# Optimization experiments

Measured on AMD Instinct MI355X. Metric: run time of the kernel, lower is better.

## Reference

```python
import jax, jax.numpy as jnp
import numpy as np

B, IN, E, H, MO, OUT, K = 32768, 512, 8, 128, 256, 2, 2


def setup_inputs() -> dict:
    key = jax.random.key(0)
    ks = jax.random.split(key, 9)
    g = lambda k, shape, fan: (jax.random.normal(k, shape, jnp.float32) / np.sqrt(fan)).astype(jnp.float32)
    return {
        "num_prop": jax.random.normal(ks[0], (B, IN), jnp.float32),
        "cat_prop": jax.random.normal(ks[1], (B, 3), jnp.float32),
        "w_gate": g(ks[2], (IN, E), IN),
        "W1": g(ks[3], (E, IN, H), IN),
        "b1": jnp.zeros((E, H), jnp.float32),
        "W2": g(ks[4], (E, H, MO), H),
        "b2": jnp.zeros((E, MO), jnp.float32),
        "Wout": g(ks[5], (MO, OUT), MO),
        "bout": jnp.zeros((OUT,), jnp.float32),
    }


def _cv_squared(v):
    # torch.var is unbiased (ddof=1); eps = 1e-10
    return jnp.var(v, ddof=1) / (jnp.mean(v) ** 2 + 1e-10)


def reference(num_prop, cat_prop, w_gate, W1, b1, W2, b2, Wout, bout):
    b = num_prop.shape[0]
    x = num_prop  # eval mode: dropout is identity, gating noise disabled
    # --- top-k gating ---
    logits = x @ w_gate                                   # [B, E]
    top_vals, top_idx = jax.lax.top_k(logits, K)          # [B, K]
    gate_vals = jax.nn.softmax(top_vals, axis=-1)         # softmax over top-k logits
    gates = jnp.zeros_like(logits).at[jnp.arange(b)[:, None], top_idx].add(gate_vals)  # [B, E]
    # --- load-balancing loss ---
    importance = gates.sum(axis=0)                        # [E]
    load = (gates > 0).astype(jnp.float32).sum(axis=0)    # [E]
    loss = (_cv_squared(importance) + _cv_squared(load)) * 1e-2
    # --- experts (dense-equivalent: gates zero out non-selected experts) ---
    h = jax.nn.relu(jnp.einsum('bi,eih->beh', x, W1) + b1)          # [B, E, H]
    eo = jax.nn.softmax(jnp.einsum('beh,ehm->bem', h, W2) + b2, axis=-1)  # [B, E, MO]
    y = jnp.einsum('be,bem->bm', gates, eo)               # [B, MO]
    # --- output head ---
    out = y @ Wout + bout                                 # [B, OUT]
    return out, loss
```

## Files before the change

### kernel.cpp

```cpp
#include <hip/hip_runtime.h>

#define BN 32768
#define IN 512
#define NE 8
#define NH 128
#define MO 256

typedef const __attribute__((address_space(1))) unsigned int gu32;
typedef __attribute__((address_space(3))) unsigned int lu32;
typedef __attribute__((ext_vector_type(8))) short bf16x8;
typedef __attribute__((ext_vector_type(4))) float f32x4;

__device__ __forceinline__ void cp16(const float* g, float* l) {
    __builtin_amdgcn_global_load_lds((gu32*)g, (lu32*)l, 16, 0, 0);
}

__device__ __forceinline__ unsigned short f2bf(float f) {
    unsigned int u = __float_as_uint(f);
    u = (u + 0x7fffu + ((u >> 16) & 1u)) >> 16;
    return (unsigned short)u;
}
__device__ __forceinline__ float bf2f(unsigned short h) {
    return __uint_as_float((unsigned int)h << 16);
}

__global__ __launch_bounds__(256) void gate_kernel(
    const float* __restrict__ x, const float* __restrict__ wg,
    int* __restrict__ gcount, int* __restrict__ gload, float* __restrict__ gimp,
    int* __restrict__ idx_list, float* __restrict__ gate_list,
    float* __restrict__ out, const float* __restrict__ bout)
{
    __shared__ double wgt[NE][514];
    __shared__ int counts_s[NE];
    __shared__ int load_s[NE];
    __shared__ float imp_s[NE];
    __shared__ int base_s[NE];
    __shared__ int rec_e[64];
    __shared__ int rec_p[64];
    __shared__ float rec_g[64];

    int tid = threadIdx.x;
    if (tid < NE) { counts_s[tid] = 0; load_s[tid] = 0; imp_s[tid] = 0.f; }
    if (tid < 64) {
        int row = blockIdx.x * 32 + (tid >> 1);
        out[row * 2 + (tid & 1)] = bout[tid & 1];
    }
    for (int i = tid; i < IN * NE; i += 256) {
        wgt[i & 7][i >> 3] = (double)wg[i];
    }
    __syncthreads();

    int r = tid >> 3;
    int e = tid & 7;
    int row = blockIdx.x * 32 + r;

    const float4* x4 = (const float4*)(x + (size_t)row * IN);
    const double* wrow = &wgt[e][0];
    double a0 = 0.0, a1 = 0.0, a2 = 0.0, a3 = 0.0;
    #pragma unroll 8
    for (int j = 0; j < 128; ++j) {
        float4 xv = x4[j];
        const double2* wd = (const double2*)(wrow + 4 * j);
        double2 w0 = wd[0];
        double2 w1 = wd[1];
        a0 = fma((double)xv.x, w0.x, a0);
        a1 = fma((double)xv.y, w0.y, a1);
        a2 = fma((double)xv.z, w1.x, a2);
        a3 = fma((double)xv.w, w1.y, a3);
    }
    double acc = (a0 + a1) + (a2 + a3);

    double v0 = acc; int e0 = e;
    #pragma unroll
    for (int m = 1; m < 8; m <<= 1) {
        double vo = __shfl_xor(v0, m, 64);
        int    eo = __shfl_xor(e0, m, 64);
        if (vo > v0 || (vo == v0 && eo < e0)) { v0 = vo; e0 = eo; }
    }
    double v1 = (e == e0) ? -1.0e300 : acc; int e1 = e;
    #pragma unroll
    for (int m = 1; m < 8; m <<= 1) {
        double vo = __shfl_xor(v1, m, 64);
        int    eo = __shfl_xor(e1, m, 64);
        if (vo > v1 || (vo == v1 && eo < e1)) { v1 = vo; e1 = eo; }
    }

    if ((tid & 7) == 0) {
        float t1 = expf((float)(v1 - v0));
        float s = 1.f + t1;
        float g0 = 1.f / s;
        float g1 = t1 / s;
        atomicAdd(&imp_s[e0], g0);
        atomicAdd(&imp_s[e1], g1);
        if (g0 > 0.f) atomicAdd(&load_s[e0], 1);
        if (g1 > 0.f) atomicAdd(&load_s[e1], 1);
        int p0 = atomicAdd(&counts_s[e0], 1);
        int p1 = atomicAdd(&counts_s[e1], 1);
        int rl = r * 2;
        rec_e[rl] = e0; rec_e[rl + 1] = e1;
        rec_g[rl] = g0; rec_g[rl + 1] = g1;
        rec_p[rl] = p0; rec_p[rl + 1] = p1;
    }
    __syncthreads();
    if (tid < NE) {
        base_s[tid] = atomicAdd(&gcount[tid], counts_s[tid]);
        atomicAdd(&gimp[tid], imp_s[tid]);
        atomicAdd(&gload[tid], load_s[tid]);
    }
    __syncthreads();
    if (tid < 64) {
        int ee = rec_e[tid];
        int pos = base_s[ee] + rec_p[tid];
        int rw = blockIdx.x * 32 + (tid >> 1);
        idx_list[ee * BN + pos] = rw;
        gate_list[ee * BN + pos] = rec_g[tid];
    }
}

__global__ void loss_kernel(const float* __restrict__ gimp, const int* __restrict__ gload,
                            float* __restrict__ out) {
    if (threadIdx.x == 0 && blockIdx.x == 0) {
        float mi = 0.f, ml = 0.f;
        for (int e = 0; e < NE; ++e) { mi += gimp[e]; ml += (float)gload[e]; }
        mi *= 0.125f; ml *= 0.125f;
        float vi = 0.f, vl = 0.f;
        for (int e = 0; e < NE; ++e) {
            float d = gimp[e] - mi;  vi += d * d;
            float d2 = (float)gload[e] - ml; vl += d2 * d2;
        }
        vi *= (1.f / 7.f); vl *= (1.f / 7.f);
        float loss = (vi / (mi * mi + 1e-10f) + vl / (ml * ml + 1e-10f)) * 0.01f;
        out[BN * 2] = loss;
    }
}

__global__ __launch_bounds__(256) void prep_kernel(
    const float* __restrict__ W1, const float* __restrict__ W2,
    float* __restrict__ W1F, float* __restrict__ W2F)
{
    __shared__ __align__(16) char pb[32768];
    int t = threadIdx.x, b = blockIdx.x;
    if (b < 64) {
        int e = b >> 3, kt = b & 7;
        const float* src = W1 + ((size_t)e * IN + kt * 64) * NH;
        #pragma unroll
        for (int p = 0; p < 8; ++p) {
            int li = p * 256 + t;
            float4 q = *(const float4*)(src + li * 4);
            int kl = li >> 5, n0 = (li & 31) * 4;
            int ks = kl >> 5, g = (kl >> 3) & 3, kb = (kl & 7) * 2;
            float vv[4] = {q.x, q.y, q.z, q.w};
            #pragma unroll
            for (int j = 0; j < 4; ++j) {
                int n = n0 + j;
                int off = (((ks * 8 + (n >> 4)) * 64) + (n & 15) + 16 * g) * 16 + kb;
                unsigned short hh = f2bf(vv[j]);
                unsigned short hl = f2bf(vv[j] - bf2f(hh));
                *(unsigned short*)(pb + off) = hh;
                *(unsigned short*)(pb + 16384 + off) = hl;
            }
        }
        __syncthreads();
        float* dst = W1F + (size_t)b * 8192;
        #pragma unroll
        for (int p = 0; p < 8; ++p) {
            int li = p * 256 + t;
            *(int4*)(dst + li * 4) = *(const int4*)(pb + li * 16);
        }
    } else if (b < 96) {
        int bi = b - 64;
        int e = bi >> 2, kt = bi & 3;
        const float* src = W2 + ((size_t)e * NH + kt * 32) * MO;
        #pragma unroll
        for (int p = 0; p < 8; ++p) {
            int li = p * 256 + t;
            float4 q = *(const float4*)(src + li * 4);
            int kl = li >> 6, n0 = (li & 63) * 4;
            int g = kl >> 3, kb = (kl & 7) * 2;
            float vv[4] = {q.x, q.y, q.z, q.w};
            #pragma unroll
            for (int j = 0; j < 4; ++j) {
                int n = n0 + j;
                int off = ((n >> 4) * 64 + (n & 15) + 16 * g) * 16 + kb;
                unsigned short hh = f2bf(vv[j]);
                unsigned short hl = f2bf(vv[j] - bf2f(hh));
                *(unsigned short*)(pb + off) = hh;
                *(unsigned short*)(pb + 16384 + off) = hl;
            }
        }
        __syncthreads();
        float* dst = W2F + (size_t)bi * 8192;
        #pragma unroll
        for (int p = 0; p < 8; ++p) {
            int li = p * 256 + t;
            *(int4*)(dst + li * 4) = *(const int4*)(pb + li * 16);
        }
    }
}

#define OFF_AH 0
#define OFF_AL 8192
#define OFF_B1 16384
#define OFF_HH 0
#define OFF_HL 16384
#define OFF_B2 32768

__global__ __launch_bounds__(256, 2) void expert_kernel(
    const float* __restrict__ x,
    const float* __restrict__ b1, const float* __restrict__ b2,
    const float* __restrict__ Wout,
    const float* __restrict__ W1F, const float* __restrict__ W2F,
    const int* __restrict__ gcount,
    const int* __restrict__ idx_list, const float* __restrict__ gate_list,
    float* __restrict__ out)
{
    __shared__ __align__(16) char smx[66560];
    __shared__ float woutS[512];

    int e = blockIdx.y;
    int cnt = gcount[e];
    int row0 = blockIdx.x * 64;
    if (row0 >= cnt) return;
    int t = threadIdx.x;
    int l = t & 63, w = t >> 6;

    woutS[t] = Wout[t];
    woutS[256 + t] = Wout[256 + t];

    int s_mf = t >> 6;
    int s_r  = t & 15;
    int s_g  = (t >> 4) & 3;
    int rloc = s_mf * 16 + s_r;
    int sgi = row0 + rloc; if (sgi >= cnt) sgi = cnt - 1;
    const float* xrow = x + (size_t)idx_list[e * BN + sgi] * IN;

    int mbase = (w & 1) * 2;
    int nsel  = w >> 1;

    f32x4 acc1[2][4] = {};
    for (int kt = 0; kt < 8; ++kt) {
        {
            const float* gb = W1F + (size_t)(e * 8 + kt) * 8192;
            float* lb = (float*)(smx + OFF_B1);
            #pragma unroll
            for (int p = 0; p < 8; ++p)
                cp16(gb + (p * 256 + t) * 4, lb + (p * 256 + t) * 4);
        }
        #pragma unroll
        for (int ks = 0; ks < 2; ++ks) {
            int k = kt * 64 + ks * 32 + s_g * 8;
            float4 qa = *(const float4*)(xrow + k);
            float4 qb = *(const float4*)(xrow + k + 4);
            float vv[8] = {qa.x, qa.y, qa.z, qa.w, qb.x, qb.y, qb.z, qb.w};
            unsigned int dh[4], dl[4];
            #pragma unroll
            for (int j = 0; j < 4; ++j) {
                unsigned short h0 = f2bf(vv[2 * j]);
                unsigned short h1 = f2bf(vv[2 * j + 1]);
                unsigned short l0 = f2bf(vv[2 * j] - bf2f(h0));
                unsigned short l1 = f2bf(vv[2 * j + 1] - bf2f(h1));
                dh[j] = (unsigned int)h0 | ((unsigned int)h1 << 16);
                dl[j] = (unsigned int)l0 | ((unsigned int)l1 << 16);
            }
            int slot = ((ks * 4 + s_mf) * 64 + (s_r + 16 * s_g)) * 16;
            *(int4*)(smx + OFF_AH + slot) = make_int4(dh[0], dh[1], dh[2], dh[3]);
            *(int4*)(smx + OFF_AL + slot) = make_int4(dl[0], dl[1], dl[2], dl[3]);
        }
        __syncthreads();
        #pragma unroll
        for (int ks = 0; ks < 2; ++ks) {
            bf16x8 ah[2], al[2];
            #pragma unroll
            for (int mf = 0; mf < 2; ++mf) {
                int ao = ((ks * 4 + mbase + mf) * 64 + l) * 16;
                ah[mf] = *(const bf16x8*)(smx + OFF_AH + ao);
                al[mf] = *(const bf16x8*)(smx + OFF_AL + ao);
            }
            #pragma unroll
            for (int nf = 0; nf < 4; ++nf) {
                int bo = ((ks * 8 + nsel * 4 + nf) * 64 + l) * 16;
                bf16x8 bh = *(const bf16x8*)(smx + OFF_B1 + bo);
                bf16x8 bl = *(const bf16x8*)(smx + OFF_B1 + 16384 + bo);
                #pragma unroll
                for (int mf = 0; mf < 2; ++mf) {
                    acc1[mf][nf] = __builtin_amdgcn_mfma_f32_16x16x32_bf16(ah[mf], bh, acc1[mf][nf], 0, 0, 0);
                    acc1[mf][nf] = __builtin_amdgcn_mfma_f32_16x16x32_bf16(ah[mf], bl, acc1[mf][nf], 0, 0, 0);
                    acc1[mf][nf] = __builtin_amdgcn_mfma_f32_16x16x32_bf16(al[mf], bh, acc1[mf][nf], 0, 0, 0);
                    acc1[mf][nf] = __builtin_amdgcn_mfma_f32_16x16x32_bf16(al[mf], bl, acc1[mf][nf], 0, 0, 0);
                }
            }
        }
        __syncthreads();
    }

    #pragma unroll
    for (int mf = 0; mf < 2; ++mf) {
        int mf2 = (w & 1) * 2 + mf;
        int rlow = 4 * (l >> 4);
        #pragma unroll
        for (int nf = 0; nf < 4; ++nf) {
            int c = nsel * 64 + nf * 16 + (l & 15);
            float b1v = b1[e * NH + c];
            int ks2 = c >> 5;
            int g2 = (c >> 3) & 3;
            int boff = ((ks2 * 4 + mf2) * 64) * 16 + (c & 7) * 2;
            #pragma unroll
            for (int rg = 0; rg < 4; ++rg) {
                float v = fmaxf(acc1[mf][nf][rg] + b1v, 0.f);
                unsigned short hh = f2bf(v);
                unsigned short hl = f2bf(v - bf2f(hh));
                int off = boff + ((rlow + rg) + 16 * g2) * 16;
                *(unsigned short*)(smx + OFF_HH + off) = hh;
                *(unsigned short*)(smx + OFF_HL + off) = hl;
            }
        }
    }
    __syncthreads();

    f32x4 acc2[2][8] = {};
    for (int kt2 = 0; kt2 < 4; ++kt2) {
        {
            const float* gb = W2F + (size_t)(e * 4 + kt2) * 8192;
            float* lb = (float*)(smx + OFF_B2);
            #pragma unroll
            for (int p = 0; p < 8; ++p)
                cp16(gb + (p * 256 + t) * 4, lb + (p * 256 + t) * 4);
        }
        __syncthreads();
        bf16x8 ah[2], al[2];
        #pragma unroll
        for (int mf = 0; mf < 2; ++mf) {
            int ao = ((kt2 * 4 + mbase + mf) * 64 + l) * 16;
            ah[mf] = *(const bf16x8*)(smx + OFF_HH + ao);
            al[mf] = *(const bf16x8*)(smx + OFF_HL + ao);
        }
        #pragma unroll
        for (int nf = 0; nf < 8; ++nf) {
            int bo = ((nsel * 8 + nf) * 64 + l) * 16;
            bf16x8 bh = *(const bf16x8*)(smx + OFF_B2 + bo);
            bf16x8 bl = *(const bf16x8*)(smx + OFF_B2 + 16384 + bo);
            #pragma unroll
            for (int mf = 0; mf < 2; ++mf) {
                acc2[mf][nf] = __builtin_amdgcn_mfma_f32_16x16x32_bf16(ah[mf], bh, acc2[mf][nf], 0, 0, 0);
                acc2[mf][nf] = __builtin_amdgcn_mfma_f32_16x16x32_bf16(ah[mf], bl, acc2[mf][nf], 0, 0, 0);
                acc2[mf][nf] = __builtin_amdgcn_mfma_f32_16x16x32_bf16(al[mf], bh, acc2[mf][nf], 0, 0, 0);
                acc2[mf][nf] = __builtin_amdgcn_mfma_f32_16x16x32_bf16(al[mf], bl, acc2[mf][nf], 0, 0, 0);
            }
        }
        __syncthreads();
    }

    float* zl = (float*)smx;
    #pragma unroll
    for (int mf = 0; mf < 2; ++mf) {
        int rbase = (w & 1) * 32 + mf * 16 + 4 * (l >> 4);
        #pragma unroll
        for (int nf = 0; nf < 8; ++nf) {
            int c = nsel * 128 + nf * 16 + (l & 15);
            float b2v = b2[e * MO + c];
            #pragma unroll
            for (int rg = 0; rg < 4; ++rg)
                zl[(rbase + rg) * 260 + c] = acc2[mf][nf][rg] + b2v;
        }
    }
    __syncthreads();

    int rr = w * 16 + (l >> 2);
    int c0 = l & 3;
    float vreg[64];
    float m = -1e30f;
    #pragma unroll
    for (int j = 0; j < 64; ++j) {
        vreg[j] = zl[rr * 260 + c0 + 4 * j];
        m = fmaxf(m, vreg[j]);
    }
    m = fmaxf(m, __shfl_xor(m, 1, 64));
    m = fmaxf(m, __shfl_xor(m, 2, 64));
    float s = 0.f, o0 = 0.f, o1 = 0.f;
    #pragma unroll
    for (int j = 0; j < 64; ++j) {
        float tt = __expf(vreg[j] - m);
        s += tt;
        float2 wv = *(const float2*)&woutS[(c0 + 4 * j) * 2];
        o0 = fmaf(tt, wv.x, o0);
        o1 = fmaf(tt, wv.y, o1);
    }
    s  += __shfl_xor(s, 1, 64);  s  += __shfl_xor(s, 2, 64);
    o0 += __shfl_xor(o0, 1, 64); o0 += __shfl_xor(o0, 2, 64);
    o1 += __shfl_xor(o1, 1, 64); o1 += __shfl_xor(o1, 2, 64);
    if (c0 == 0) {
        int gi = row0 + rr;
        if (gi < cnt) {
            float g = gate_list[e * BN + gi];
            int brow = idx_list[e * BN + gi];
            float inv = 1.f / s;
            atomicAdd(&out[brow * 2 + 0], g * o0 * inv);
            atomicAdd(&out[brow * 2 + 1], g * o1 * inv);
        }
    }
}

extern "C" void kernel_launch(void* const* d_in, const int* in_sizes, int n_in,
                              void* d_out, int out_size, void* d_ws, size_t ws_size,
                              hipStream_t stream) {
    const float* x    = (const float*)d_in[0];
    const float* wg   = (const float*)d_in[2];
    const float* W1   = (const float*)d_in[3];
    const float* b1   = (const float*)d_in[4];
    const float* W2   = (const float*)d_in[5];
    const float* b2   = (const float*)d_in[6];
    const float* Wout = (const float*)d_in[7];
    const float* bout = (const float*)d_in[8];
    float* out = (float*)d_out;

    char* ws = (char*)d_ws;
    int*   gcount    = (int*)(ws + 0);
    int*   gload     = (int*)(ws + 32);
    float* gimp      = (float*)(ws + 64);
    int*   idx_list  = (int*)(ws + 128);
    float* gate_list = (float*)(ws + 128 + sizeof(int) * NE * BN);
    float* W1F       = (float*)(ws + 128 + 8 * NE * BN);
    float* W2F       = (float*)(ws + 128 + 8 * NE * BN + 64 * 32768);

    hipMemsetAsync(ws, 0, 128, stream);
    prep_kernel<<<96, 256, 0, stream>>>(W1, W2, W1F, W2F);
    gate_kernel<<<BN / 32, 256, 0, stream>>>(x, wg, gcount, gload, gimp,
                                             idx_list, gate_list, out, bout);
    loss_kernel<<<1, 64, 0, stream>>>(gimp, gload, out);
    dim3 eg(BN / 64, NE);
    expert_kernel<<<eg, 256, 0, stream>>>(x, b1, b2, Wout, W1F, W2F,
                                          gcount, idx_list, gate_list, out);
}
```

Measured before the change: 228.0 us.

## Compute gating logits with split-bf16 MFMA, FP64 fallback for near-ties; fold loss into expert kernel

The gate kernel now computes logits with split-bf16 MFMA (hi/lo parts, three products) instead of per-thread FP64 dot products, covering 64 rows per block. When the 2nd and 3rd logits are within a small margin, it recomputes that row in FP64 so the top-2 selection still matches. The separate loss kernel is removed and its work done by one thread of the expert kernel, saving a launch. The risks are divergent slow paths when near-ties occur, and the tie threshold being too small to catch every MFMA rounding error.

```diff
diff --git a/kernel.cpp b/kernel.cpp
--- a/kernel.cpp
+++ b/kernel.cpp
@@ -30,76 +30,135 @@
     int* __restrict__ idx_list, float* __restrict__ gate_list,
     float* __restrict__ out, const float* __restrict__ bout)
 {
-    __shared__ double wgt[NE][514];
+    __shared__ __align__(16) char wb[32768];
     __shared__ int counts_s[NE];
     __shared__ int load_s[NE];
     __shared__ float imp_s[NE];
     __shared__ int base_s[NE];
-    __shared__ int rec_e[64];
-    __shared__ int rec_p[64];
-    __shared__ float rec_g[64];
+    __shared__ int rec_e[128];
+    __shared__ int rec_p[128];
+    __shared__ float rec_g[128];
 
     int tid = threadIdx.x;
     if (tid < NE) { counts_s[tid] = 0; load_s[tid] = 0; imp_s[tid] = 0.f; }
-    if (tid < 64) {
-        int row = blockIdx.x * 32 + (tid >> 1);
+    if (tid < 128) {
+        int row = blockIdx.x * 64 + (tid >> 1);
         out[row * 2 + (tid & 1)] = bout[tid & 1];
     }
-    for (int i = tid; i < IN * NE; i += 256) {
-        wgt[i & 7][i >> 3] = (double)wg[i];
+    for (int idx = tid; idx < 1024; idx += 256) {
+        int ks = idx >> 6, ls = idx & 63;
+        int col = ls & 15;
+        int kb = 32 * ks + 8 * (ls >> 4);
+        unsigned int ph[4], pl[4];
+        #pragma unroll
+        for (int j = 0; j < 4; ++j) {
+            float v0 = (col < 8) ? wg[(kb + 2 * j) * NE + col] : 0.f;
+            float v1 = (col < 8) ? wg[(kb + 2 * j + 1) * NE + col] : 0.f;
+            unsigned short h0 = f2bf(v0), h1 = f2bf(v1);
+            unsigned short l0 = f2bf(v0 - bf2f(h0)), l1 = f2bf(v1 - bf2f(h1));
+            ph[j] = (unsigned int)h0 | ((unsigned int)h1 << 16);
+            pl[j] = (unsigned int)l0 | ((unsigned int)l1 << 16);
+        }
+        *(int4*)(wb + ks * 1024 + ls * 16) = make_int4(ph[0], ph[1], ph[2], ph[3]);
+        *(int4*)(wb + 16384 + ks * 1024 + ls * 16) = make_int4(pl[0], pl[1], pl[2], pl[3]);
     }
     __syncthreads();
 
-    int r = tid >> 3;
-    int e = tid & 7;
-    int row = blockIdx.x * 32 + r;
-
-    const float4* x4 = (const float4*)(x + (size_t)row * IN);
-    const double* wrow = &wgt[e][0];
-    double a0 = 0.0, a1 = 0.0, a2 = 0.0, a3 = 0.0;
-    #pragma unroll 8
-    for (int j = 0; j < 128; ++j) {
-        float4 xv = x4[j];
-        const double2* wd = (const double2*)(wrow + 4 * j);
-        double2 w0 = wd[0];
-        double2 w1 = wd[1];
-        a0 = fma((double)xv.x, w0.x, a0);
-        a1 = fma((double)xv.y, w0.y, a1);
-        a2 = fma((double)xv.z, w1.x, a2);
-        a3 = fma((double)xv.w, w1.y, a3);
-    }
-    double acc = (a0 + a1) + (a2 + a3);
-
-    double v0 = acc; int e0 = e;
-    #pragma unroll
-    for (int m = 1; m < 8; m <<= 1) {
-        double vo = __shfl_xor(v0, m, 64);
-        int    eo = __shfl_xor(e0, m, 64);
-        if (vo > v0 || (vo == v0 && eo < e0)) { v0 = vo; e0 = eo; }
-    }
-    double v1 = (e == e0) ? -1.0e300 : acc; int e1 = e;
-    #pragma unroll
-    for (int m = 1; m < 8; m <<= 1) {
-        double vo = __shfl_xor(v1, m, 64);
-        int    eo = __shfl_xor(e1, m, 64);
-        if (vo > v1 || (vo == v1 && eo < e1)) { v1 = vo; e1 = eo; }
-    }
-
-    if ((tid & 7) == 0) {
-        float t1 = expf((float)(v1 - v0));
-        float s = 1.f + t1;
-        float g0 = 1.f / s;
-        float g1 = t1 / s;
-        atomicAdd(&imp_s[e0], g0);
-        atomicAdd(&imp_s[e1], g1);
-        if (g0 > 0.f) atomicAdd(&load_s[e0], 1);
-        if (g1 > 0.f) atomicAdd(&load_s[e1], 1);
-        int p0 = atomicAdd(&counts_s[e0], 1);
-        int p1 = atomicAdd(&counts_s[e1], 1);
-        int rl = r * 2;
-        rec_e[rl] = e0; rec_e[rl + 1] = e1;
-        rec_g[rl] = g0; rec_g[rl + 1] = g1;
-        rec_p[rl] = p0; rec_p[rl + 1] = p1;
+    int w = tid >> 6, l = tid & 63;
+    int e = l & 15;
+    int rowA = blockIdx.x * 64 + w * 16 + e;
+    const float* px = x + (size_t)rowA * IN + 8 * (l >> 4);
+
+    f32x4 acc = {};
+    #pragma unroll
+    for (int ks = 0; ks < 16; ++ks) {
+        float4 qa = *(const float4*)(px + 32 * ks);
+        float4 qb = *(const float4*)(px + 32 * ks + 4);
+        float v[8] = {qa.x, qa.y, qa.z, qa.w, qb.x, qb.y, qb.z, qb.w};
+        bf16x8 ah, al;
+        #pragma unroll
+        for (int i = 0; i < 8; ++i) {
+            unsigned short h = f2bf(v[i]);
+            ah[i] = (short)h;
+            al[i] = (short)f2bf(v[i] - bf2f(h));
+        }
+        bf16x8 bh = *(const bf16x8*)(wb + ks * 1024 + l * 16);
+        bf16x8 bl = *(const bf16x8*)(wb + 16384 + ks * 1024 + l * 16);
+        acc = __builtin_amdgcn_mfma_f32_16x16x32_bf16(ah, bh, acc, 0, 0, 0);
+        acc = __builtin_amdgcn_mfma_f32_16x16x32_bf16(ah, bl, acc, 0, 0, 0);
+        acc = __builtin_amdgcn_mfma_f32_16x16x32_bf16(al, bh, acc, 0, 0, 0);
+    }
+
+    #pragma unroll
+    for (int reg = 0; reg < 4; ++reg) {
+        int rloc = w * 16 + 4 * (l >> 4) + reg;
+        int row = blockIdx.x * 64 + rloc;
+        float lv = (e < 8) ? acc[reg] : -1e30f;
+
+        float v0 = lv; int e0 = e;
+        #pragma unroll
+        for (int m = 1; m < 8; m <<= 1) {
+            float vo = __shfl_xor(v0, m, 64);
+            int eo = __shfl_xor(e0, m, 64);
+            if (vo > v0 || (vo == v0 && eo < e0)) { v0 = vo; e0 = eo; }
+        }
+        float v1 = (e == e0 || e >= 8) ? -1e30f : lv; int e1 = e;
+        #pragma unroll
+        for (int m = 1; m < 8; m <<= 1) {
+            float vo = __shfl_xor(v1, m, 64);
+            int eo = __shfl_xor(e1, m, 64);
+            if (vo > v1 || (vo == v1 && eo < e1)) { v1 = vo; e1 = eo; }
+        }
+        float v2 = (e == e0 || e == e1 || e >= 8) ? -1e30f : lv;
+        #pragma unroll
+        for (int m = 1; m < 8; m <<= 1) v2 = fmaxf(v2, __shfl_xor(v2, m, 64));
+
+        double dv0 = v0, dv1 = v1;
+        int f0 = e0, f1 = e1;
+        if (e < 8 && v1 - v2 < 2e-4f) {
+            const float* xr = x + (size_t)row * IN;
+            double d0 = 0, d1 = 0, d2 = 0, d3 = 0;
+            for (int k = 0; k < IN; k += 4) {
+                float4 xv = *(const float4*)(xr + k);
+                d0 = fma((double)xv.x, (double)wg[(k    ) * NE + e], d0);
+                d1 = fma((double)xv.y, (double)wg[(k + 1) * NE + e], d1);
+                d2 = fma((double)xv.z, (double)wg[(k + 2) * NE + e], d2);
+                d3 = fma((double)xv.w, (double)wg[(k + 3) * NE + e], d3);
+            }
+            double ad = (d0 + d1) + (d2 + d3);
+            double w0 = ad; int g0i = e;
+            #pragma unroll
+            for (int m = 1; m < 8; m <<= 1) {
+                double vo = __shfl_xor(w0, m, 64);
+                int eo = __shfl_xor(g0i, m, 64);
+                if (vo > w0 || (vo == w0 && eo < g0i)) { w0 = vo; g0i = eo; }
+            }
+            double w1 = (e == g0i) ? -1.0e300 : ad; int g1i = e;
+            #pragma unroll
+            for (int m = 1; m < 8; m <<= 1) {
+                double vo = __shfl_xor(w1, m, 64);
+                int eo = __shfl_xor(g1i, m, 64);
+                if (vo > w1 || (vo == w1 && eo < g1i)) { w1 = vo; g1i = eo; }
+            }
+            dv0 = w0; dv1 = w1; f0 = g0i; f1 = g1i;
+        }
+
+        if (e == 0) {
+            float t1 = expf((float)(dv1 - dv0));
+            float s = 1.f + t1;
+            float g0 = 1.f / s;
+            float g1 = t1 / s;
+            atomicAdd(&imp_s[f0], g0);
+            atomicAdd(&imp_s[f1], g1);
+            if (g0 > 0.f) atomicAdd(&load_s[f0], 1);
+            if (g1 > 0.f) atomicAdd(&load_s[f1], 1);
+            int p0 = atomicAdd(&counts_s[f0], 1);
+            int p1 = atomicAdd(&counts_s[f1], 1);
+            int rl = rloc * 2;
+            rec_e[rl] = f0; rec_e[rl + 1] = f1;
+            rec_g[rl] = g0; rec_g[rl + 1] = g1;
+            rec_p[rl] = p0; rec_p[rl + 1] = p1;
+        }
     }
     __syncthreads();
     if (tid < NE) {
@@ -108,29 +167,12 @@
         atomicAdd(&gload[tid], load_s[tid]);
     }
     __syncthreads();
-    if (tid < 64) {
+    if (tid < 128) {
         int ee = rec_e[tid];
         int pos = base_s[ee] + rec_p[tid];
-        int rw = blockIdx.x * 32 + (tid >> 1);
+        int rw = blockIdx.x * 64 + (tid >> 1);
         idx_list[ee * BN + pos] = rw;
         gate_list[ee * BN + pos] = rec_g[tid];
-    }
-}
-
-__global__ void loss_kernel(const float* __restrict__ gimp, const int* __restrict__ gload,
-                            float* __restrict__ out) {
-    if (threadIdx.x == 0 && blockIdx.x == 0) {
-        float mi = 0.f, ml = 0.f;
-        for (int e = 0; e < NE; ++e) { mi += gimp[e]; ml += (float)gload[e]; }
-        mi *= 0.125f; ml *= 0.125f;
-        float vi = 0.f, vl = 0.f;
-        for (int e = 0; e < NE; ++e) {
-            float d = gimp[e] - mi;  vi += d * d;
-            float d2 = (float)gload[e] - ml; vl += d2 * d2;
-        }
-        vi *= (1.f / 7.f); vl *= (1.f / 7.f);
-        float loss = (vi / (mi * mi + 1e-10f) + vl / (ml * ml + 1e-10f)) * 0.01f;
-        out[BN * 2] = loss;
     }
 }
 
@@ -211,6 +253,7 @@
     const float* __restrict__ Wout,
     const float* __restrict__ W1F, const float* __restrict__ W2F,
     const int* __restrict__ gcount,
+    const float* __restrict__ gimp, const int* __restrict__ gload,
     const int* __restrict__ idx_list, const float* __restrict__ gate_list,
     float* __restrict__ out)
 {
@@ -220,6 +263,18 @@
     int e = blockIdx.y;
     int cnt = gcount[e];
     int row0 = blockIdx.x * 64;
+    if (e == 0 && blockIdx.x == 0 && threadIdx.x == 0) {
+        float mi = 0.f, ml = 0.f;
+        for (int k = 0; k < NE; ++k) { mi += gimp[k]; ml += (float)gload[k]; }
+        mi *= 0.125f; ml *= 0.125f;
+        float vi = 0.f, vl = 0.f;
+        for (int k = 0; k < NE; ++k) {
+            float d = gimp[k] - mi;  vi += d * d;
+            float d2 = (float)gload[k] - ml; vl += d2 * d2;
+        }
+        vi *= (1.f / 7.f); vl *= (1.f / 7.f);
+        out[BN * 2] = (vi / (mi * mi + 1e-10f) + vl / (ml * ml + 1e-10f)) * 0.01f;
+    }
     if (row0 >= cnt) return;
     int t = threadIdx.x;
     int l = t & 63, w = t >> 6;
@@ -330,7 +385,7 @@
         bf16x8 ah[2], al[2];
         #pragma unroll
         for (int mf = 0; mf < 2; ++mf) {
-            int ao = ((kt2 * 4 + mbase + mf) * 64 + l) * 16;
+            int ao = ((kt2 * 4 + (w & 1) * 2 + mf) * 64 + l) * 16;
             ah[mf] = *(const bf16x8*)(smx + OFF_HH + ao);
             al[mf] = *(const bf16x8*)(smx + OFF_HL + ao);
         }
@@ -424,10 +479,10 @@
 
     hipMemsetAsync(ws, 0, 128, stream);
     prep_kernel<<<96, 256, 0, stream>>>(W1, W2, W1F, W2F);
-    gate_kernel<<<BN / 32, 256, 0, stream>>>(x, wg, gcount, gload, gimp,
+    gate_kernel<<<BN / 64, 256, 0, stream>>>(x, wg, gcount, gload, gimp,
                                              idx_list, gate_list, out, bout);
-    loss_kernel<<<1, 64, 0, stream>>>(gimp, gload, out);
     dim3 eg(BN / 64, NE);
     expert_kernel<<<eg, 256, 0, stream>>>(x, b1, b2, Wout, W1F, W2F,
-                                          gcount, idx_list, gate_list, out);
-}
+                                          gcount, gimp, gload,
+                                          idx_list, gate_list, out);
+}
```

Measured after the change: 216.6 us. 1.05x faster.
